# Performance work log

Hardware: AMD Instinct MI355X
Metric: run time of the kernel (lower is better)

## Reference

```python
import jax, jax.numpy as jnp
import numpy as np

B, S, H = 2, 2048, 2048
NH, HD = 16, 128
TS = 512
RATE = 0.1          # custom_active_rate (used as the sampled mean, deterministic)
ALPHA = 0.5         # ts_ema_alpha
EPS = 1e-6
BASE = 10000.0
K_IDX = int((1.0 - RATE) * TS)   # torch.kthvalue k (1-indexed k-th smallest) = 460


def _rmsnorm(x, w):
    xf = x.astype(jnp.float32)
    var = jnp.mean(xf * xf, axis=-1, keepdims=True)
    return (xf * jax.lax.rsqrt(var + EPS)).astype(x.dtype) * w


def _rope_tables():
    inv = 1.0 / (BASE ** (np.arange(0, HD, 2, dtype=np.float32) / HD))
    t = np.arange(S, dtype=np.float32)
    freqs = np.outer(t, inv)                       # [S, HD/2]
    emb = np.concatenate([freqs, freqs], axis=-1)  # [S, HD]
    return jnp.asarray(np.cos(emb)), jnp.asarray(np.sin(emb))


def _rotate_half(x):
    x1, x2 = jnp.split(x, 2, axis=-1)
    return jnp.concatenate([-x2, x1], axis=-1)


def setup_inputs() -> dict:
    key = jax.random.key(0)
    ks = jax.random.split(key, 9)
    sc = 0.02
    return {
        'hidden_states': jax.random.normal(ks[0], (B, S, H), jnp.float32),
        'last_layer_ts_embedding': jax.random.normal(ks[1], (B, S, TS), jnp.float32),
        'Wq': jax.random.normal(ks[2], (H, H), jnp.float32) * sc,
        'Wk': jax.random.normal(ks[3], (H, H), jnp.float32) * sc,
        'Wv': jax.random.normal(ks[4], (H, H), jnp.float32) * sc,
        'Wo': jax.random.normal(ks[5], (H, H), jnp.float32) * sc,
        'Wts': jax.random.normal(ks[6], (H, TS), jnp.float32) * sc,
        'ts_norm_w': jnp.ones((TS,), jnp.float32),
        'Worig': jax.random.normal(ks[7], (TS, 3 * H), jnp.float32) * sc,
    }


def reference(hidden_states, last_layer_ts_embedding, Wq, Wk, Wv, Wo, Wts, ts_norm_w, Worig):
    # --- custom TS gating path ---
    ts = hidden_states @ Wts                                  # [B,S,TS]
    ts = (1.0 - ALPHA) * ts + ALPHA * last_layer_ts_embedding # EMA with previous layer
    ts = _rmsnorm(ts, ts_norm_w)
    # torch.kthvalue: k-th smallest along last dim, keepdim
    kth = jnp.sort(ts, axis=-1)[..., K_IDX - 1:K_IDX]          # [B,S,1]
    ts_filtered = jax.nn.relu(ts - kth)
    origin = ts_filtered @ Worig                               # [B,S,3H]
    q_add = origin[..., :H]
    k_add = origin[..., H:2 * H]
    v_add = k_add                                              # 'qkv' mode: v uses split[1]

    # --- qkv projections (llama linear, no bias) ---
    q = hidden_states @ Wq + q_add
    k = hidden_states @ Wk + k_add
    v = hidden_states @ Wv + v_add
    q = q.reshape(B, S, NH, HD).transpose(0, 2, 1, 3)          # [B,NH,S,HD]
    k = k.reshape(B, S, NH, HD).transpose(0, 2, 1, 3)
    v = v.reshape(B, S, NH, HD).transpose(0, 2, 1, 3)

    # --- rotary embedding ---
    cos, sin = _rope_tables()                                  # [S,HD]
    cos = cos[None, None]; sin = sin[None, None]
    q = q * cos + _rotate_half(q) * sin
    k = k * cos + _rotate_half(k) * sin

    # --- eager attention: QK^T, causal mask add, fp32 softmax, PV ---
    scores = jnp.einsum('bhqd,bhkd->bhqk', q, k) / jnp.sqrt(jnp.float32(HD))
    causal = jnp.tril(jnp.ones((S, S), bool))
    mask = jnp.where(causal, 0.0, -1e9).astype(scores.dtype)[None, None]
    probs = jax.nn.softmax((scores + mask).astype(jnp.float32), axis=-1).astype(q.dtype)
    attn = jnp.einsum('bhqk,bhkd->bhqd', probs, v)
    attn = attn.transpose(0, 2, 1, 3).reshape(B, S, H)
    return attn @ Wo
```

## Files before the change

### kernel.cpp

```cpp
#include <hip/hip_runtime.h>
#include <cstdint>

typedef __bf16 bf16_t;
typedef __bf16 bf16x8 __attribute__((ext_vector_type(8)));
typedef __bf16 bf16x4 __attribute__((ext_vector_type(4)));
typedef float  f32x4  __attribute__((ext_vector_type(4)));
typedef bf16x8 __attribute__((may_alias)) bf16x8a;
typedef bf16x4 __attribute__((may_alias)) bf16x4a;
typedef f32x4  __attribute__((may_alias)) f32x4a;

#define S_LEN 2048
#define HDIM  2048
#define NHEAD 16
#define HD    128
#define TSD   512
#define BROWS 4096
#define KIDX  459

__device__ __forceinline__ f32x4 mfma_bf16(bf16x8 a, bf16x8 b, f32x4 c) {
  return __builtin_amdgcn_mfma_f32_16x16x32_bf16(a, b, c, 0, 0, 0);
}

__device__ __forceinline__ void gld_lds16(const bf16_t* g, bf16_t* l) {
  __builtin_amdgcn_global_load_lds(
      (__attribute__((address_space(1))) void*)(void*)const_cast<bf16_t*>(g),
      (__attribute__((address_space(3))) void*)(void*)(l), 16, 0, 0);
}

__device__ __forceinline__ uint32_t pk2(float a, float b) {
  union { bf16_t h; uint16_t u; } ua, ub;
  ua.h = (bf16_t)a; ub.h = (bf16_t)b;
  return (uint32_t)ua.u | ((uint32_t)ub.u << 16);
}

__global__ void k_cvt(const float* __restrict__ in, bf16_t* __restrict__ out, int n) {
  int i = (blockIdx.x * 256 + threadIdx.x) * 4;
  if (i >= n) return;
  f32x4 v = *(const f32x4a*)(in + i);
  bf16x4 o = { (bf16_t)v.x, (bf16_t)v.y, (bf16_t)v.z, (bf16_t)v.w };
  *(bf16x4a*)(out + i) = o;
}

__global__ void k_transpose(const float* __restrict__ in, bf16_t* __restrict__ out,
                            int R, int C, int ldin) {
  __shared__ float tile[32][33];
  int c0 = blockIdx.x * 32, r0 = blockIdx.y * 32;
  int tx = threadIdx.x, ty = threadIdx.y;
  for (int i = ty; i < 32; i += 8)
    tile[i][tx] = in[(size_t)(r0 + i) * ldin + c0 + tx];
  __syncthreads();
  for (int i = ty; i < 32; i += 8)
    out[(size_t)(c0 + i) * R + r0 + tx] = (bf16_t)tile[tx][i];
}

__global__ void k_vtrans(const bf16_t* __restrict__ in, bf16_t* __restrict__ out) {
  __shared__ bf16_t t[64][72];
  int s0 = blockIdx.x * 64, d0 = blockIdx.y * 64, bh = blockIdx.z;
  const bf16_t* src = in + (size_t)bh * S_LEN * HD;
  bf16_t* dst = out + (size_t)bh * HD * S_LEN;
  int tid = threadIdx.x;
  for (int g = tid; g < 512; g += 256) {
    int r = g >> 3, cc = g & 7;
    *(bf16x8a*)&t[r][cc * 8] = *(const bf16x8a*)(src + (size_t)(s0 + r) * HD + d0 + cc * 8);
  }
  __syncthreads();
  for (int g = tid; g < 512; g += 256) {
    int dr = g >> 3, sc = g & 7;
    bf16x8 v;
#pragma unroll
    for (int j = 0; j < 8; j++) v[j] = t[sc * 8 + j][dr];
    *(bf16x8a*)(dst + (size_t)(d0 + dr) * S_LEN + s0 + sc * 8) = v;
  }
}

template<int MODE>
__global__ __launch_bounds__(256)
void k_gemm(const bf16_t* __restrict__ A, const bf16_t* __restrict__ Bt,
            float* __restrict__ outF, bf16_t* __restrict__ outB,
            const bf16_t* __restrict__ addend, int M, int N, int K,
            int addLd, int addCol)
{
  __shared__ __align__(16) bf16_t As[128 * 32];
  __shared__ __align__(16) bf16_t Bs[128 * 32];
  const int tid  = threadIdx.x;
  const int lane = tid & 63, w = tid >> 6;
  const int quad = lane >> 4, l15 = lane & 15;
  const int m0 = blockIdx.y * 128, n0 = blockIdx.x * 128;
  const int wm = (w >> 1) * 64, wn = (w & 1) * 64;

  f32x4 acc[4][4];
#pragma unroll
  for (int i = 0; i < 4; i++)
#pragma unroll
    for (int j = 0; j < 4; j++) { f32x4 z = {0.f,0.f,0.f,0.f}; acc[i][j] = z; }

  const int srow = w * 16 + (lane >> 2);
  const int scol = (lane & 3) * 8;

  for (int k0 = 0; k0 < K; k0 += 32) {
    __syncthreads();
    gld_lds16(A  + (size_t)(m0 +      srow) * K + k0 + scol, As + (size_t)w * 512);
    gld_lds16(A  + (size_t)(m0 + 64 + srow) * K + k0 + scol, As + (size_t)(4 + w) * 512);
    gld_lds16(Bt + (size_t)(n0 +      srow) * K + k0 + scol, Bs + (size_t)w * 512);
    gld_lds16(Bt + (size_t)(n0 + 64 + srow) * K + k0 + scol, Bs + (size_t)(4 + w) * 512);
    __syncthreads();
    bf16x8 af[4], bv[4];
#pragma unroll
    for (int i = 0; i < 4; i++)
      af[i] = *(const bf16x8a*)&As[(wm + i * 16 + l15) * 32 + quad * 8];
#pragma unroll
    for (int j = 0; j < 4; j++)
      bv[j] = *(const bf16x8a*)&Bs[(wn + j * 16 + l15) * 32 + quad * 8];
#pragma unroll
    for (int i = 0; i < 4; i++)
#pragma unroll
      for (int j = 0; j < 4; j++)
        acc[i][j] = mfma_bf16(af[i], bv[j], acc[i][j]);
  }

#pragma unroll
  for (int i = 0; i < 4; i++)
#pragma unroll
    for (int j = 0; j < 4; j++)
#pragma unroll
      for (int r = 0; r < 4; r++) {
        int row = m0 + wm + i * 16 + quad * 4 + r;
        int col = n0 + wn + j * 16 + l15;
        float v = acc[i][j][r];
        if (MODE == 0) {
          outF[(size_t)row * N + col] = v;
        } else if (MODE == 1) {
          outB[(size_t)row * N + col] = (bf16_t)v;
        } else {
          v += (float)addend[(size_t)row * addLd + addCol + col];
          int s = row & (S_LEN - 1), b = row >> 11;
          int h = col >> 7, d = col & (HD - 1);
          outB[(((size_t)(b * NHEAD + h) * S_LEN) + s) * HD + d] = (bf16_t)v;
        }
      }
}

__global__ __launch_bounds__(256)
void k_tsproc(const float* __restrict__ ts, const float* __restrict__ lte,
              const float* __restrict__ wn, bf16_t* __restrict__ tsf)
{
  __shared__ float sv[TSD];
  __shared__ float red[4];
  int row = blockIdx.x;
  int t = threadIdx.x;
  const float* tr = ts  + (size_t)row * TSD;
  const float* lr = lte + (size_t)row * TSD;
  float v0 = 0.5f * tr[t] + 0.5f * lr[t];
  float v1 = 0.5f * tr[t + 256] + 0.5f * lr[t + 256];
  float ss = v0 * v0 + v1 * v1;
#pragma unroll
  for (int o = 32; o > 0; o >>= 1) ss += __shfl_down(ss, o);
  int lane = t & 63, wv = t >> 6;
  if (lane == 0) red[wv] = ss;
  __syncthreads();
  float tot = red[0] + red[1] + red[2] + red[3];
  float scl = rsqrtf(tot * (1.0f / TSD) + 1e-6f);
  float n0 = v0 * scl * wn[t];
  float n1 = v1 * scl * wn[t + 256];
  sv[t] = n0; sv[t + 256] = n1;
  __syncthreads();
  for (int k = 2; k <= TSD; k <<= 1) {
    for (int j = k >> 1; j > 0; j >>= 1) {
#pragma unroll
      for (int u = 0; u < 2; u++) {
        int idx = t + u * 256;
        int ixj = idx ^ j;
        if (ixj > idx) {
          float a = sv[idx], b = sv[ixj];
          bool up = ((idx & k) == 0);
          if ((a > b) == up) { sv[idx] = b; sv[ixj] = a; }
        }
      }
      __syncthreads();
    }
  }
  float kth = sv[KIDX];
  tsf[(size_t)row * TSD + t]       = (bf16_t)fmaxf(n0 - kth, 0.0f);
  tsf[(size_t)row * TSD + t + 256] = (bf16_t)fmaxf(n1 - kth, 0.0f);
}

__global__ void k_ropetab(float* __restrict__ tabC, float* __restrict__ tabS) {
  int gid = blockIdx.x * 256 + threadIdx.x;
  int d = gid & 63, s = gid >> 6;
  float inv = powf(10000.0f, (float)(-2 * d) * (1.0f / 128.0f));
  float sn, c;
  sincosf((float)s * inv, &sn, &c);
  tabC[gid] = c; tabS[gid] = sn;
}

__global__ void k_rope(bf16_t* __restrict__ x, const float* __restrict__ tabC,
                       const float* __restrict__ tabS) {
  int gid = blockIdx.x * 256 + threadIdx.x;
  int d = gid & 63;
  int rowi = gid >> 6;
  int s = rowi & (S_LEN - 1);
  bf16_t* p = x + (size_t)rowi * HD;
  float c  = tabC[s * 64 + d];
  float sn = tabS[s * 64 + d];
  float x0 = (float)p[d], x1 = (float)p[d + 64];
  p[d]      = (bf16_t)(x0 * c - x1 * sn);
  p[d + 64] = (bf16_t)(x1 * c + x0 * sn);
}

__global__ __launch_bounds__(256, 4)
void k_attn(const bf16_t* __restrict__ qb, const bf16_t* __restrict__ kb,
            const bf16_t* __restrict__ vtb, bf16_t* __restrict__ attnB)
{
  __shared__ __align__(16) bf16_t Kt[64 * 128];
  __shared__ __align__(16) bf16_t Vt[128 * 64];

  const int bid = blockIdx.x;
  const int bh  = (bid & 7) + 8 * (bid >> 8);
  static const int qmap[32] = {31,0,30,1,29,2,28,3,27,4,26,5,25,6,24,7,
                               23,8,22,9,21,10,20,11,19,12,18,13,17,14,16,15};
  const int q0 = qmap[((bid >> 3) + (bid >> 8)) & 31] * 64;

  const int tid = threadIdx.x;
  const int lane = tid & 63, w = tid >> 6;
  const int quad = lane >> 4, l15 = lane & 15;

  const bf16_t* Q  = qb  + (size_t)bh * S_LEN * HD;
  const bf16_t* Kg = kb  + (size_t)bh * S_LEN * HD;
  const bf16_t* Vg = vtb + (size_t)bh * HD * S_LEN;

  bf16x8 qf[4];
  {
    const bf16_t* qrow = Q + (size_t)(q0 + w * 16 + l15) * HD;
#pragma unroll
    for (int c = 0; c < 4; c++)
      qf[c] = *(const bf16x8a*)(qrow + c * 32 + quad * 8);
  }

  int kfo[4];
#pragma unroll
  for (int c = 0; c < 4; c++)
    kfo[c] = l15 * 128 + (((c * 4 + quad) ^ (l15 & 7)) * 8);
  int vfo[2];
#pragma unroll
  for (int kc = 0; kc < 2; kc++)
    vfo[kc] = l15 * 64 + (((kc * 4 + quad) ^ (l15 & 7)) * 8);

  int kSrc[4], vSrc[4];
#pragma unroll
  for (int j = 0; j < 4; j++) {
    int G  = (w * 4 + j) * 64 + lane;
    int r  = G >> 4, gl = G & 15;
    kSrc[j] = r * HD + ((gl ^ (r & 7)) * 8);
    int d  = G >> 3, vg = G & 7;
    vSrc[j] = d * S_LEN + ((vg ^ (d & 7)) * 8);
  }

  const int addrA = 4 * (l15 + 32 * (quad & 1));
  const int addrB = addrA + 64;
  const bool selHi = (quad >> 1) != 0;

  f32x4 o[8];
#pragma unroll
  for (int t8 = 0; t8 < 8; t8++) { f32x4 z = {0.f,0.f,0.f,0.f}; o[t8] = z; }
  float m_i = -1e30f, l_i = 0.0f;

  const float scale = 0.08838834764831845f;
  const int kEnd = q0;
  const int qrow_i = q0 + w * 16 + l15;

  for (int k0 = 0; k0 <= kEnd; k0 += 64) {
    {
      const bf16_t* Kgk = Kg + (size_t)k0 * HD;
      const bf16_t* Vgk = Vg + k0;
#pragma unroll
      for (int j = 0; j < 4; j++)
        gld_lds16(Kgk + kSrc[j], Kt + (w * 4 + j) * 512);
#pragma unroll
      for (int j = 0; j < 4; j++)
        gld_lds16(Vgk + vSrc[j], Vt + (w * 4 + j) * 512);
    }
    __syncthreads();

    f32x4 st_[4];
#pragma unroll
    for (int nt = 0; nt < 4; nt++) { f32x4 z = {0.f,0.f,0.f,0.f}; st_[nt] = z; }
    __builtin_amdgcn_s_setprio(1);
#pragma unroll
    for (int nt = 0; nt < 4; nt++)
#pragma unroll
      for (int c = 0; c < 4; c++) {
        bf16x8 kf = *(const bf16x8a*)(Kt + kfo[c] + nt * 2048);
        st_[nt] = mfma_bf16(kf, qf[c], st_[nt]);
      }
    __builtin_amdgcn_s_setprio(0);

    if (k0 == q0) {
#pragma unroll
      for (int nt = 0; nt < 4; nt++)
#pragma unroll
        for (int r = 0; r < 4; r++) {
          int key = k0 + nt * 16 + quad * 4 + r;
          float v = st_[nt][r] * scale;
          st_[nt][r] = (key > qrow_i) ? -1e9f : v;
        }
    } else {
#pragma unroll
      for (int nt = 0; nt < 4; nt++)
#pragma unroll
        for (int r = 0; r < 4; r++)
          st_[nt][r] *= scale;
    }

    float mx = st_[0][0];
#pragma unroll
    for (int nt = 0; nt < 4; nt++)
#pragma unroll
      for (int r = 0; r < 4; r++) mx = fmaxf(mx, st_[nt][r]);
    mx = fmaxf(mx, __shfl_xor(mx, 16));
    mx = fmaxf(mx, __shfl_xor(mx, 32));

    if (__ballot(mx > m_i + 8.0f)) {
      float mnew = fmaxf(m_i, mx);
      float alpha = __expf(m_i - mnew);
      m_i = mnew;
      l_i *= alpha;
#pragma unroll
      for (int t8 = 0; t8 < 8; t8++)
#pragma unroll
        for (int r = 0; r < 4; r++)
          o[t8][r] *= alpha;
    }

    float rs = 0.0f;
#pragma unroll
    for (int nt = 0; nt < 4; nt++)
#pragma unroll
      for (int r = 0; r < 4; r++) {
        float pv = __expf(st_[nt][r] - m_i);
        st_[nt][r] = pv;
        rs += pv;
      }
    rs += __shfl_xor(rs, 16);
    rs += __shfl_xor(rs, 32);
    l_i += rs;

    uint32_t pk[4][2];
#pragma unroll
    for (int nt = 0; nt < 4; nt++) {
      pk[nt][0] = pk2(st_[nt][0], st_[nt][1]);
      pk[nt][1] = pk2(st_[nt][2], st_[nt][3]);
    }

#pragma unroll
    for (int kc = 0; kc < 2; kc++) {
      uint32_t a0 = __builtin_amdgcn_ds_bpermute(addrA, (int)pk[2*kc][0]);
      uint32_t a1 = __builtin_amdgcn_ds_bpermute(addrA, (int)pk[2*kc][1]);
      uint32_t a2 = __builtin_amdgcn_ds_bpermute(addrB, (int)pk[2*kc][0]);
      uint32_t a3 = __builtin_amdgcn_ds_bpermute(addrB, (int)pk[2*kc][1]);
      uint32_t b0 = __builtin_amdgcn_ds_bpermute(addrA, (int)pk[2*kc+1][0]);
      uint32_t b1 = __builtin_amdgcn_ds_bpermute(addrA, (int)pk[2*kc+1][1]);
      uint32_t b2 = __builtin_amdgcn_ds_bpermute(addrB, (int)pk[2*kc+1][0]);
      uint32_t b3 = __builtin_amdgcn_ds_bpermute(addrB, (int)pk[2*kc+1][1]);
      union { bf16x8 v; uint32_t d[4]; } pf;
      pf.d[0] = selHi ? b0 : a0;
      pf.d[1] = selHi ? b1 : a1;
      pf.d[2] = selHi ? b2 : a2;
      pf.d[3] = selHi ? b3 : a3;
      __builtin_amdgcn_s_setprio(1);
#pragma unroll
      for (int t8 = 0; t8 < 8; t8++) {
        bf16x8 vf = *(const bf16x8a*)(Vt + vfo[kc] + t8 * 1024);
        o[t8] = mfma_bf16(vf, pf.v, o[t8]);
      }
      __builtin_amdgcn_s_setprio(0);
    }

    __syncthreads();
  }

  const int b = bh >> 4, h = bh & 15;
  const float rl = 1.0f / l_i;
  uint32_t* outp = (uint32_t*)(attnB + (size_t)(b * S_LEN + qrow_i) * HDIM + h * HD);
#pragma unroll
  for (int t8 = 0; t8 < 8; t8++)
#pragma unroll
    for (int pr = 0; pr < 2; pr++) {
      uint32_t v = pk2(o[t8][2*pr] * rl, o[t8][2*pr+1] * rl);
      outp[t8 * 8 + quad * 2 + pr] = v;
    }
}

extern "C" void kernel_launch(void* const* d_in, const int* in_sizes, int n_in,
                              void* d_out, int out_size, void* d_ws, size_t ws_size,
                              hipStream_t stream) {
  const float* hs    = (const float*)d_in[0];
  const float* lte   = (const float*)d_in[1];
  const float* Wq    = (const float*)d_in[2];
  const float* Wk    = (const float*)d_in[3];
  const float* Wv    = (const float*)d_in[4];
  const float* Wo    = (const float*)d_in[5];
  const float* Wts   = (const float*)d_in[6];
  const float* tsw   = (const float*)d_in[7];
  const float* Worig = (const float*)d_in[8];
  float* out = (float*)d_out;

  char* p = (char*)d_ws;
  bf16_t* hsB   = (bf16_t*)(p);
  bf16_t* wT    = (bf16_t*)(p + 16777216);
  float*  tsB   = (float*)(p + 25165824);
  bf16_t* tsf   = (bf16_t*)(p + 33554432);
  bf16_t* qkadd = (bf16_t*)(p + 37748736);
  bf16_t* attnB = qkadd;
  bf16_t* vtb   = (bf16_t*)(p + 54525952);
  bf16_t* qbuf  = (bf16_t*)(p + 71303168);
  bf16_t* kbuf  = (bf16_t*)(p + 88080384);
  bf16_t* vbuf  = (bf16_t*)(p + 104857600);
  float*  tabC  = tsB;
  float*  tabS  = tsB + 131072;

  k_cvt<<<8192, 256, 0, stream>>>(hs, hsB, BROWS * HDIM);
  k_transpose<<<dim3(16, 64), dim3(32, 8), 0, stream>>>(Wts, wT, 2048, 512, 512);
  k_gemm<0><<<dim3(4, 32), 256, 0, stream>>>(hsB, wT, tsB, nullptr, nullptr,
                                             4096, 512, 2048, 0, 0);
  k_tsproc<<<4096, 256, 0, stream>>>(tsB, lte, tsw, tsf);
  k_ropetab<<<512, 256, 0, stream>>>(tabC, tabS);
  k_transpose<<<dim3(128, 16), dim3(32, 8), 0, stream>>>(Worig, wT, 512, 4096, 6144);
  k_gemm<1><<<dim3(32, 32), 256, 0, stream>>>(tsf, wT, nullptr, qkadd, nullptr,
                                              4096, 4096, 512, 0, 0);
  k_transpose<<<dim3(64, 64), dim3(32, 8), 0, stream>>>(Wq, wT, 2048, 2048, 2048);
  k_gemm<2><<<dim3(16, 32), 256, 0, stream>>>(hsB, wT, nullptr, qbuf, qkadd,
                                              4096, 2048, 2048, 4096, 0);
  k_transpose<<<dim3(64, 64), dim3(32, 8), 0, stream>>>(Wk, wT, 2048, 2048, 2048);
  k_gemm<2><<<dim3(16, 32), 256, 0, stream>>>(hsB, wT, nullptr, kbuf, qkadd,
                                              4096, 2048, 2048, 4096, 2048);
  k_transpose<<<dim3(64, 64), dim3(32, 8), 0, stream>>>(Wv, wT, 2048, 2048, 2048);
  k_gemm<2><<<dim3(16, 32), 256, 0, stream>>>(hsB, wT, nullptr, vbuf, qkadd,
                                              4096, 2048, 2048, 4096, 2048);
  k_rope<<<16384, 256, 0, stream>>>(qbuf, tabC, tabS);
  k_rope<<<16384, 256, 0, stream>>>(kbuf, tabC, tabS);
  k_vtrans<<<dim3(32, 2, 32), 256, 0, stream>>>(vbuf, vtb);
  k_transpose<<<dim3(64, 64), dim3(32, 8), 0, stream>>>(Wo, wT, 2048, 2048, 2048);
  k_attn<<<1024, 256, 0, stream>>>(qbuf, kbuf, vtb, attnB);
  k_gemm<0><<<dim3(16, 32), 256, 0, stream>>>(attnB, wT, out, nullptr, nullptr,
                                              4096, 2048, 2048, 0, 0);
}
```

Measured before the change: 630.1 us.

## Fuse QKV projections with TS-origin add and RoPE into one concatenated-K GEMM

Concatenates each projection weight with its slice of Worig along K (2048+512), so q/k/v = [hs | ts_filtered] @ [W ; Worig_slice] runs as a single batched GEMM launch covering all three outputs. This removes the separate origin GEMM, the qkadd intermediate buffer and its reread, and the two standalone RoPE kernels. RoPE is applied in the epilogue by reassigning output columns so each warp holds both d and d+64. It costs six transpose launches to build the concatenated weights and adds some redundant MMA work, since the k and v halves of Worig are multiplied twice.

```diff
diff --git a/kernel.cpp b/kernel.cpp
--- a/kernel.cpp
+++ b/kernel.cpp
@@ -16,6 +16,7 @@
 #define TSD   512
 #define BROWS 4096
 #define KIDX  459
+#define KCAT  2560
 
 __device__ __forceinline__ f32x4 mfma_bf16(bf16x8 a, bf16x8 b, f32x4 c) {
   return __builtin_amdgcn_mfma_f32_16x16x32_bf16(a, b, c, 0, 0, 0);
@@ -42,7 +43,7 @@
 }
 
 __global__ void k_transpose(const float* __restrict__ in, bf16_t* __restrict__ out,
-                            int R, int C, int ldin) {
+                            int ldin, int ldout, int koff) {
   __shared__ float tile[32][33];
   int c0 = blockIdx.x * 32, r0 = blockIdx.y * 32;
   int tx = threadIdx.x, ty = threadIdx.y;
@@ -50,7 +51,7 @@
     tile[i][tx] = in[(size_t)(r0 + i) * ldin + c0 + tx];
   __syncthreads();
   for (int i = ty; i < 32; i += 8)
-    out[(size_t)(c0 + i) * R + r0 + tx] = (bf16_t)tile[tx][i];
+    out[(size_t)(c0 + i) * ldout + koff + r0 + tx] = (bf16_t)tile[tx][i];
 }
 
 __global__ void k_vtrans(const bf16_t* __restrict__ in, bf16_t* __restrict__ out) {
@@ -73,12 +74,9 @@
   }
 }
 
-template<int MODE>
 __global__ __launch_bounds__(256)
 void k_gemm(const bf16_t* __restrict__ A, const bf16_t* __restrict__ Bt,
-            float* __restrict__ outF, bf16_t* __restrict__ outB,
-            const bf16_t* __restrict__ addend, int M, int N, int K,
-            int addLd, int addCol)
+            float* __restrict__ outF, int M, int N, int K)
 {
   __shared__ __align__(16) bf16_t As[128 * 32];
   __shared__ __align__(16) bf16_t Bs[128 * 32];
@@ -126,18 +124,98 @@
       for (int r = 0; r < 4; r++) {
         int row = m0 + wm + i * 16 + quad * 4 + r;
         int col = n0 + wn + j * 16 + l15;
-        float v = acc[i][j][r];
-        if (MODE == 0) {
-          outF[(size_t)row * N + col] = v;
-        } else if (MODE == 1) {
-          outB[(size_t)row * N + col] = (bf16_t)v;
-        } else {
-          v += (float)addend[(size_t)row * addLd + addCol + col];
-          int s = row & (S_LEN - 1), b = row >> 11;
-          int h = col >> 7, d = col & (HD - 1);
-          outB[(((size_t)(b * NHEAD + h) * S_LEN) + s) * HD + d] = (bf16_t)v;
+        outF[(size_t)row * N + col] = acc[i][j][r];
+      }
+}
+
+__global__ __launch_bounds__(256)
+void k_gemm_qkv(const bf16_t* __restrict__ hsB, const bf16_t* __restrict__ tsf,
+                const bf16_t* __restrict__ wcat, bf16_t* __restrict__ outQKV,
+                const float* __restrict__ tabC, const float* __restrict__ tabS)
+{
+  __shared__ __align__(16) bf16_t As[128 * 32];
+  __shared__ __align__(16) bf16_t Bs[128 * 32];
+  const int tid  = threadIdx.x;
+  const int lane = tid & 63, w = tid >> 6;
+  const int quad = lane >> 4, l15 = lane & 15;
+  const int wi = blockIdx.x >> 4;
+  const int n0 = (blockIdx.x & 15) * 128;
+  const int m0 = blockIdx.y * 128;
+  const int wm = (w >> 1) * 64;
+  const bf16_t* Bt = wcat + (size_t)wi * HDIM * KCAT;
+  bf16_t* outp = outQKV + (size_t)wi * 8388608;
+
+  int col2[4];
+#pragma unroll
+  for (int j = 0; j < 4; j++)
+    col2[j] = (w & 1) * 32 + (j & 1) * 16 + (j >> 1) * 64 + l15;
+
+  f32x4 acc[4][4];
+#pragma unroll
+  for (int i = 0; i < 4; i++)
+#pragma unroll
+    for (int j = 0; j < 4; j++) { f32x4 z = {0.f,0.f,0.f,0.f}; acc[i][j] = z; }
+
+  const int srow = w * 16 + (lane >> 2);
+  const int scol = (lane & 3) * 8;
+
+  for (int k0 = 0; k0 < KCAT; k0 += 32) {
+    const bf16_t* Ab; int lda, kc;
+    if (k0 < HDIM) { Ab = hsB; lda = HDIM; kc = k0; }
+    else           { Ab = tsf; lda = TSD;  kc = k0 - HDIM; }
+    __syncthreads();
+    gld_lds16(Ab + (size_t)(m0 +      srow) * lda + kc + scol, As + (size_t)w * 512);
+    gld_lds16(Ab + (size_t)(m0 + 64 + srow) * lda + kc + scol, As + (size_t)(4 + w) * 512);
+    gld_lds16(Bt + (size_t)(n0 +      srow) * KCAT + k0 + scol, Bs + (size_t)w * 512);
+    gld_lds16(Bt + (size_t)(n0 + 64 + srow) * KCAT + k0 + scol, Bs + (size_t)(4 + w) * 512);
+    __syncthreads();
+    bf16x8 af[4], bv[4];
+#pragma unroll
+    for (int i = 0; i < 4; i++)
+      af[i] = *(const bf16x8a*)&As[(wm + i * 16 + l15) * 32 + quad * 8];
+#pragma unroll
+    for (int j = 0; j < 4; j++)
+      bv[j] = *(const bf16x8a*)&Bs[col2[j] * 32 + quad * 8];
+#pragma unroll
+    for (int i = 0; i < 4; i++)
+#pragma unroll
+      for (int j = 0; j < 4; j++)
+        acc[i][j] = mfma_bf16(af[i], bv[j], acc[i][j]);
+  }
+
+  const int h = n0 >> 7;
+  if (wi == 2) {
+#pragma unroll
+    for (int i = 0; i < 4; i++)
+#pragma unroll
+      for (int r = 0; r < 4; r++) {
+        int row = m0 + wm + i * 16 + quad * 4 + r;
+        int s = row & (S_LEN - 1), b = row >> 11;
+        size_t obase = (((size_t)(b * NHEAD + h) * S_LEN) + s) * HD;
+#pragma unroll
+        for (int j = 0; j < 4; j++)
+          outp[obase + col2[j]] = (bf16_t)acc[i][j][r];
+      }
+  } else {
+#pragma unroll
+    for (int i = 0; i < 4; i++)
+#pragma unroll
+      for (int r = 0; r < 4; r++) {
+        int row = m0 + wm + i * 16 + quad * 4 + r;
+        int s = row & (S_LEN - 1), b = row >> 11;
+        size_t obase = (((size_t)(b * NHEAD + h) * S_LEN) + s) * HD;
+#pragma unroll
+        for (int j = 0; j < 2; j++) {
+          int d = (w & 1) * 32 + j * 16 + l15;
+          float lo = acc[i][j][r];
+          float hi = acc[i][j + 2][r];
+          float c  = tabC[s * 64 + d];
+          float sn = tabS[s * 64 + d];
+          outp[obase + d]      = (bf16_t)(lo * c - hi * sn);
+          outp[obase + d + 64] = (bf16_t)(hi * c + lo * sn);
         }
       }
+  }
 }
 
 __global__ __launch_bounds__(256)
@@ -191,20 +269,6 @@
   float sn, c;
   sincosf((float)s * inv, &sn, &c);
   tabC[gid] = c; tabS[gid] = sn;
-}
-
-__global__ void k_rope(bf16_t* __restrict__ x, const float* __restrict__ tabC,
-                       const float* __restrict__ tabS) {
-  int gid = blockIdx.x * 256 + threadIdx.x;
-  int d = gid & 63;
-  int rowi = gid >> 6;
-  int s = rowi & (S_LEN - 1);
-  bf16_t* p = x + (size_t)rowi * HD;
-  float c  = tabC[s * 64 + d];
-  float sn = tabS[s * 64 + d];
-  float x0 = (float)p[d], x1 = (float)p[d + 64];
-  p[d]      = (bf16_t)(x0 * c - x1 * sn);
-  p[d + 64] = (bf16_t)(x1 * c + x0 * sn);
 }
 
 __global__ __launch_bounds__(256, 4)
@@ -409,38 +473,32 @@
   bf16_t* wT    = (bf16_t*)(p + 16777216);
   float*  tsB   = (float*)(p + 25165824);
   bf16_t* tsf   = (bf16_t*)(p + 33554432);
-  bf16_t* qkadd = (bf16_t*)(p + 37748736);
-  bf16_t* attnB = qkadd;
+  bf16_t* wcat  = (bf16_t*)(p + 37748736);
+  bf16_t* attnB = (bf16_t*)(p + 37748736);
   bf16_t* vtb   = (bf16_t*)(p + 54525952);
   bf16_t* qbuf  = (bf16_t*)(p + 71303168);
   bf16_t* kbuf  = (bf16_t*)(p + 88080384);
   bf16_t* vbuf  = (bf16_t*)(p + 104857600);
   float*  tabC  = tsB;
   float*  tabS  = tsB + 131072;
+  bf16_t* wcatQ = wcat;
+  bf16_t* wcatK = wcat + (size_t)HDIM * KCAT;
+  bf16_t* wcatV = wcat + (size_t)2 * HDIM * KCAT;
 
   k_cvt<<<8192, 256, 0, stream>>>(hs, hsB, BROWS * HDIM);
-  k_transpose<<<dim3(16, 64), dim3(32, 8), 0, stream>>>(Wts, wT, 2048, 512, 512);
-  k_gemm<0><<<dim3(4, 32), 256, 0, stream>>>(hsB, wT, tsB, nullptr, nullptr,
-                                             4096, 512, 2048, 0, 0);
+  k_transpose<<<dim3(16, 64), dim3(32, 8), 0, stream>>>(Wts, wT, 512, 2048, 0);
+  k_gemm<<<dim3(4, 32), 256, 0, stream>>>(hsB, wT, tsB, 4096, 512, 2048);
   k_tsproc<<<4096, 256, 0, stream>>>(tsB, lte, tsw, tsf);
   k_ropetab<<<512, 256, 0, stream>>>(tabC, tabS);
-  k_transpose<<<dim3(128, 16), dim3(32, 8), 0, stream>>>(Worig, wT, 512, 4096, 6144);
-  k_gemm<1><<<dim3(32, 32), 256, 0, stream>>>(tsf, wT, nullptr, qkadd, nullptr,
-                                              4096, 4096, 512, 0, 0);
-  k_transpose<<<dim3(64, 64), dim3(32, 8), 0, stream>>>(Wq, wT, 2048, 2048, 2048);
-  k_gemm<2><<<dim3(16, 32), 256, 0, stream>>>(hsB, wT, nullptr, qbuf, qkadd,
-                                              4096, 2048, 2048, 4096, 0);
-  k_transpose<<<dim3(64, 64), dim3(32, 8), 0, stream>>>(Wk, wT, 2048, 2048, 2048);
-  k_gemm<2><<<dim3(16, 32), 256, 0, stream>>>(hsB, wT, nullptr, kbuf, qkadd,
-                                              4096, 2048, 2048, 4096, 2048);
-  k_transpose<<<dim3(64, 64), dim3(32, 8), 0, stream>>>(Wv, wT, 2048, 2048, 2048);
-  k_gemm<2><<<dim3(16, 32), 256, 0, stream>>>(hsB, wT, nullptr, vbuf, qkadd,
-                                              4096, 2048, 2048, 4096, 2048);
-  k_rope<<<16384, 256, 0, stream>>>(qbuf, tabC, tabS);
-  k_rope<<<16384, 256, 0, stream>>>(kbuf, tabC, tabS);
+  k_transpose<<<dim3(64, 64), dim3(32, 8), 0, stream>>>(Wq, wcatQ, 2048, KCAT, 0);
+  k_transpose<<<dim3(64, 16), dim3(32, 8), 0, stream>>>(Worig, wcatQ, 6144, KCAT, 2048);
+  k_transpose<<<dim3(64, 64), dim3(32, 8), 0, stream>>>(Wk, wcatK, 2048, KCAT, 0);
+  k_transpose<<<dim3(64, 16), dim3(32, 8), 0, stream>>>(Worig + 2048, wcatK, 6144, KCAT, 2048);
+  k_transpose<<<dim3(64, 64), dim3(32, 8), 0, stream>>>(Wv, wcatV, 2048, KCAT, 0);
+  k_transpose<<<dim3(64, 16), dim3(32, 8), 0, stream>>>(Worig + 2048, wcatV, 6144, KCAT, 2048);
+  k_gemm_qkv<<<dim3(48, 32), 256, 0, stream>>>(hsB, tsf, wcat, qbuf, tabC, tabS);
   k_vtrans<<<dim3(32, 2, 32), 256, 0, stream>>>(vbuf, vtb);
-  k_transpose<<<dim3(64, 64), dim3(32, 8), 0, stream>>>(Wo, wT, 2048, 2048, 2048);
+  k_transpose<<<dim3(64, 64), dim3(32, 8), 0, stream>>>(Wo, wT, 2048, 2048, 0);
   k_attn<<<1024, 256, 0, stream>>>(qbuf, kbuf, vtb, attnB);
-  k_gemm<0><<<dim3(16, 32), 256, 0, stream>>>(attnB, wT, out, nullptr, nullptr,
-                                              4096, 2048, 2048, 0, 0);
-}
+  k_gemm<<<dim3(16, 32), 256, 0, stream>>>(attnB, wT, out, 4096, 2048, 2048);
+}
```

After: 603.5 us. -4.2%, faster.
